# Kernel tuning notes

Measured on AMD Instinct MI355X. Metric: run time of the kernel, lower is better.

The kernel has to match this reference:

```python
import jax, jax.numpy as jnp
import numpy as np
from jax import lax

N, C_IN, C_OUT, H, W = 8, 64, 64, 128, 128
K, KS, STRIDE, PAD, GROUPS = 4, 3, 1, 1, 1


def setup_inputs() -> dict:
    key = jax.random.key(0)
    ks = jax.random.split(key, 10)
    s = 0.05
    return {
        "x": jax.random.normal(ks[0], (N, C_IN, H, W), jnp.float32),
        "weight": jax.random.normal(ks[1], (K, C_OUT, C_IN // GROUPS, KS, KS), jnp.float32) * s,
        "conv_w": jax.random.normal(ks[2], (C_OUT, C_IN, KS, KS), jnp.float32) * s,
        "conv_b": jax.random.normal(ks[3], (C_OUT,), jnp.float32) * s,
        "net0_w": jax.random.normal(ks[4], (K, 1, 1, 1, 1), jnp.float32) * s,
        "net0_b": jax.random.normal(ks[5], (K,), jnp.float32) * s,
        "net1_w": jax.random.normal(ks[6], (K, 1, 3, 3, 3), jnp.float32) * s,
        "net1_b": jax.random.normal(ks[7], (K,), jnp.float32) * s,
        "net2_w": jax.random.normal(ks[8], (K, 1, 5, 3, 3), jnp.float32) * s,
        "net2_b": jax.random.normal(ks[9], (K,), jnp.float32) * s,
    }


def _conv3d_mean(x5, w, b, pad):
    # x5: (N,1,C,H,W); w: (K,1,kd,kh,kw); 'same'-style padding per kernel.
    y = lax.conv_general_dilated(x5, w, (1, 1, 1), [(p, p) for p in pad],
                                 dimension_numbers=('NCDHW', 'OIDHW', 'NCDHW'))
    # global avg pool over (C,H,W); bias is constant so add after the mean.
    return jnp.mean(y, axis=(2, 3, 4)) + b[None, :]


def reference(x, weight, conv_w, conv_b, net0_w, net0_b, net1_w, net1_b, net2_w, net2_b):
    dn2 = ('NCHW', 'OIHW', 'NCHW')
    # static residual conv branch
    r = lax.conv_general_dilated(x, conv_w, (STRIDE, STRIDE), [(PAD, PAD)] * 2,
                                 dimension_numbers=dn2) + conv_b[None, :, None, None]
    # attention over 3D convs of x.unsqueeze(1)
    x5 = x[:, None]  # (N,1,C,H,W)
    logits = (_conv3d_mean(x5, net0_w, net0_b, (0, 0, 0))
              + _conv3d_mean(x5, net1_w, net1_b, (1, 1, 1))
              + _conv3d_mean(x5, net2_w, net2_b, (2, 1, 1)))  # (N,K)
    att = jax.nn.softmax(logits, axis=-1)
    # per-sample dynamic kernel mixing: (N,K) @ (K,out,in/g,kh,kw)
    agg_w = jnp.einsum('nk,koihw->noihw', att, weight)
    # grouped conv with groups = GROUPS*N == per-sample conv (vmapped)
    def per_sample(xi, wi):
        return lax.conv_general_dilated(xi[None], wi, (STRIDE, STRIDE), [(PAD, PAD)] * 2,
                                        dimension_numbers=dn2,
                                        feature_group_count=GROUPS)[0]
    out = jax.vmap(per_sample)(x, agg_w)  # (N,out,H,W)
    return out + r
```

## Files before the change

### kernel.cpp

```cpp
#include <hip/hip_runtime.h>


typedef unsigned short ushort_t;
typedef __attribute__((ext_vector_type(8))) short bf16x8;
typedef __attribute__((ext_vector_type(4))) float f32x4;

__device__ __forceinline__ ushort_t f2bf(float f) {
    unsigned u = __float_as_uint(f);
    unsigned r = (u + 0x7fffu + ((u >> 16) & 1u)) >> 16;
    return (ushort_t)r;
}

__global__ __launch_bounds__(256) void kTR(const float* __restrict__ x,
                                           ushort_t* __restrict__ xt,
                                           float* __restrict__ cat) {
    int bid = blockIdx.x;
    int h = bid & 127, n = bid >> 7;
    int tid = threadIdx.x;

    __shared__ ushort_t t[128 * 72];
    __shared__ float catloc[15];
    if (tid < 15) catloc[tid] = 0.f;
    __syncthreads();

    const float* xp = x + (size_t)n * 64 * 16384 + h * 128;
    int wq = tid & 31;

#pragma unroll
    for (int i = 0; i < 8; ++i) {
        int idx = i * 256 + tid;
        int ci = idx >> 5;
        float4 v = *(const float4*)(xp + (size_t)ci * 16384 + wq * 4);

        int w0 = wq * 4;
        t[(w0 + 0) * 72 + ci] = f2bf(v.x);
        t[(w0 + 1) * 72 + ci] = f2bf(v.y);
        t[(w0 + 2) * 72 + ci] = f2bf(v.z);
        t[(w0 + 3) * 72 + ci] = f2bf(v.w);

        float s4 = v.x + v.y + v.z + v.w;
#pragma unroll
        for (int m = 1; m <= 16; m <<= 1) s4 += __shfl_xor(s4, m);
        int cd = (ci == 0) ? 0 : (ci == 1) ? 1 : (ci == 62) ? 3 : (ci == 63) ? 4 : 2;
        if (wq == 0) {
            atomicAdd(&catloc[cd * 3 + 0], s4);
            atomicAdd(&catloc[cd * 3 + 1], v.x);
        }
        if (wq == 31) atomicAdd(&catloc[cd * 3 + 2], v.w);
    }
    __syncthreads();

    ushort_t* op = xt + ((size_t)(n * 128 + h)) * 128 * 64;
#pragma unroll
    for (int j = 0; j < 4; ++j) {
        int q = j * 256 + tid;
        int w = q >> 3, ci8 = q & 7;
        uint4 v = *(const uint4*)&t[w * 72 + ci8 * 8];
        *(uint4*)(op + (size_t)w * 64 + ci8 * 8) = v;
    }

    if (tid < 15) {
        int cd = tid / 3, st = tid % 3;
        int ch = (h == 0) ? 0 : (h == 127) ? 2 : 1;
        atomicAdd(&cat[((n * 5 + cd) * 3 + ch) * 3 + st], catloc[tid]);
    }
}

__global__ __launch_bounds__(256) void kW(const float* __restrict__ cat,
                                          const float* __restrict__ nw0, const float* __restrict__ nb0,
                                          const float* __restrict__ nw1, const float* __restrict__ nb1,
                                          const float* __restrict__ nw2, const float* __restrict__ nb2,
                                          const float* __restrict__ weight,
                                          const float* __restrict__ convw,
                                          ushort_t* __restrict__ weff) {
    int n = blockIdx.x >> 2, q = blockIdx.x & 3;
    int tid = threadIdx.x;
    __shared__ float att_s[4];

    if (tid < 4) {
        int k = tid;
        float c[5][3][3];
#pragma unroll
        for (int i = 0; i < 5; ++i)
#pragma unroll
            for (int j = 0; j < 3; ++j)
#pragma unroll
                for (int s = 0; s < 3; ++s)
                    c[i][j][s] = cat[((n * 5 + i) * 3 + j) * 3 + s];

        const float invV = 1.0f / (64.f * 128.f * 128.f);
        auto box = [&](int sd, int sh, int sw) -> float {
            float acc = 0.f;
#pragma unroll
            for (int cd = 0; cd < 5; ++cd) {
                int dv = (cd == 0) ? 0 : (cd == 1) ? 1 : (cd == 3) ? 62 : (cd == 4) ? 63 : -1;
                bool incd = (dv < 0) || (dv >= sd && dv < 64 + sd);
#pragma unroll
                for (int ch = 0; ch < 3; ++ch) {
                    int hv = (ch == 0) ? 0 : (ch == 2) ? 127 : -1;
                    bool inch = (hv < 0) || (hv >= sh && hv < 128 + sh);
                    if (incd && inch) {
                        float v = c[cd][ch][0];
                        if (sw == -1) v -= c[cd][ch][2];
                        else if (sw == 1) v -= c[cd][ch][1];
                        acc += v;
                    }
                }
            }
            return acc;
        };

        float lg = nb0[k] + nb1[k] + nb2[k];
        {
            float tot = 0.f;
#pragma unroll
            for (int i = 0; i < 5; ++i)
#pragma unroll
                for (int j = 0; j < 3; ++j) tot += c[i][j][0];
            lg += nw0[k] * tot * invV;
        }
#pragma unroll
        for (int dz = 0; dz < 3; ++dz)
#pragma unroll
            for (int dy = 0; dy < 3; ++dy)
#pragma unroll
                for (int dx = 0; dx < 3; ++dx)
                    lg += nw1[k * 27 + dz * 9 + dy * 3 + dx] *
                          box(dz - 1, dy - 1, dx - 1) * invV;
#pragma unroll
        for (int dz = 0; dz < 5; ++dz)
#pragma unroll
            for (int dy = 0; dy < 3; ++dy)
#pragma unroll
                for (int dx = 0; dx < 3; ++dx)
                    lg += nw2[k * 45 + dz * 9 + dy * 3 + dx] *
                          box(dz - 2, dy - 1, dx - 1) * invV;

        float m = fmaxf(lg, __shfl_xor(lg, 1));
        m = fmaxf(m, __shfl_xor(m, 2));
        float e = __expf(lg - m);
        float ssum = e + __shfl_xor(e, 1);
        ssum += __shfl_xor(ssum, 2);
        att_s[k] = e / ssum;
    }
    __syncthreads();

    float a0 = att_s[0], a1 = att_s[1], a2 = att_s[2], a3 = att_s[3];
    int ci = tid & 63;
    int co_base = q * 16 + (tid >> 6) * 4;
#pragma unroll
    for (int p = 0; p < 4; ++p) {
        int co = co_base + p;
        const float* cw = convw + (size_t)(co * 64 + ci) * 9;
        const float* w0 = weight + (size_t)((0 * 64 + co) * 64 + ci) * 9;
        const float* w1 = weight + (size_t)((1 * 64 + co) * 64 + ci) * 9;
        const float* w2 = weight + (size_t)((2 * 64 + co) * 64 + ci) * 9;
        const float* w3 = weight + (size_t)((3 * 64 + co) * 64 + ci) * 9;
#pragma unroll
        for (int s = 0; s < 9; ++s) {
            float v = cw[s] + a0 * w0[s] + a1 * w1[s] + a2 * w2[s] + a3 * w3[s];
            weff[((size_t)(n * 9 + s) * 64 + co) * 64 + ci] = f2bf(v);
        }
    }
}

__global__ __launch_bounds__(256) void kC(const ushort_t* __restrict__ xt,
                                          const ushort_t* __restrict__ weff,
                                          const float* __restrict__ convb,
                                          float* __restrict__ out) {
    int bid = blockIdx.x;
    int wt = bid & 1;
    int hp = (bid >> 1) & 63;
    int n = bid >> 7;
    int h0 = hp * 2;
    int w0 = wt * 64;

    __shared__ __align__(16) ushort_t lds[4 * 66 * 72];

    int tid = threadIdx.x;
    int lane = tid & 63;
    int wave = tid >> 6;
    int kq = lane >> 4;
    int l15 = lane & 15;

    for (int idx = tid; idx < 2112; idx += 256) {
        int ci8 = idx & 7;
        int rc = idx >> 3;
        int c = rc % 66;
        int r = rc / 66;
        int hg = h0 + r - 1;
        int wg = w0 + c - 1;
        uint4 v = make_uint4(0u, 0u, 0u, 0u);
        if (hg >= 0 && hg < 128 && wg >= 0 && wg < 128) {
            v = *(const uint4*)(xt + (((size_t)n * 128 + hg) * 128 + wg) * 64 + ci8 * 8);
        }
        *(uint4*)&lds[(r * 66 + c) * 72 + ci8 * 8] = v;
    }

    int co_a = wave * 16 + l15;
    bf16x8 afrag[9][2];
#pragma unroll
    for (int s = 0; s < 9; ++s)
#pragma unroll
        for (int kc = 0; kc < 2; ++kc)
            afrag[s][kc] = *(const bf16x8*)(weff +
                ((size_t)((n * 9 + s) * 64 + co_a)) * 64 + kc * 32 + kq * 8);

    f32x4 acc[8];
#pragma unroll
    for (int nt = 0; nt < 8; ++nt) acc[nt] = (f32x4){0.f, 0.f, 0.f, 0.f};

    __syncthreads();

#pragma unroll
    for (int s = 0; s < 9; ++s) {
        int ky = s / 3, kx = s % 3;
#pragma unroll
        for (int kc = 0; kc < 2; ++kc) {
#pragma unroll
            for (int nt = 0; nt < 8; ++nt) {
                int r = nt >> 2;
                int wl = (nt & 3) * 16 + l15;
                bf16x8 bfrag = *(const bf16x8*)
                    &lds[((r + ky) * 66 + wl + kx) * 72 + kc * 32 + kq * 8];
                acc[nt] = __builtin_amdgcn_mfma_f32_16x16x32_bf16(
                    afrag[s][kc], bfrag, acc[nt], 0, 0, 0);
            }
        }
    }

#pragma unroll
    for (int nt = 0; nt < 8; ++nt) {
        int h = h0 + (nt >> 2);
        int w = w0 + (nt & 3) * 16 + l15;
#pragma unroll
        for (int reg = 0; reg < 4; ++reg) {
            int co = wave * 16 + kq * 4 + reg;
            float v = acc[nt][reg] + convb[co];
            out[(((size_t)n * 64 + co) * 128 + h) * 128 + w] = v;
        }
    }
}

extern "C" void kernel_launch(void* const* d_in, const int* in_sizes, int n_in,
                              void* d_out, int out_size, void* d_ws, size_t ws_size,
                              hipStream_t stream) {
    const float* x      = (const float*)d_in[0];
    const float* weight = (const float*)d_in[1];
    const float* conv_w = (const float*)d_in[2];
    const float* conv_b = (const float*)d_in[3];
    const float* n0w    = (const float*)d_in[4];
    const float* n0b    = (const float*)d_in[5];
    const float* n1w    = (const float*)d_in[6];
    const float* n1b    = (const float*)d_in[7];
    const float* n2w    = (const float*)d_in[8];
    const float* n2b    = (const float*)d_in[9];
    float* out = (float*)d_out;

    char* ws = (char*)d_ws;
    ushort_t* xt   = (ushort_t*)(ws);
    ushort_t* weff = (ushort_t*)(ws + 16777216);
    float*    cat  = (float*)(ws + 16777216 + 589824);

    hipMemsetAsync(cat, 0, 1440, stream);
    kTR<<<1024, 256, 0, stream>>>(x, xt, cat);
    kW<<<32, 256, 0, stream>>>(cat, n0w, n0b, n1w, n1b, n2w, n2b,
                               weight, conv_w, weff);
    kC<<<1024, 256, 0, stream>>>(xt, weff, conv_b, out);
}
```

Measured before the change: 143.2 us.

## Use channel-blocked bf16 layout for xt and parallelize weight mixing

The transposed input changes from NHWC to a channel-blocked [n][h][ci8][w][8] layout. The transpose kernel no longer needs an LDS staging pass, and the conv kernel's LDS tile becomes unpadded and is read with a new index pattern. The attention/weight-mixing kernel spreads the 45 box sums across threads instead of one thread per k. It also launches one block per (sample, tap) pair, which raises block count from 32 to 72. The new global read pattern in kTR (scalar loads strided by 32) and possible LDS bank conflicts in kC are the risks.

```diff
diff --git a/kernel.cpp b/kernel.cpp
--- a/kernel.cpp
+++ b/kernel.cpp
@@ -17,47 +17,49 @@
     int bid = blockIdx.x;
     int h = bid & 127, n = bid >> 7;
     int tid = threadIdx.x;
-
-    __shared__ ushort_t t[128 * 72];
+    int wg = tid & 31;
+    int ci8 = tid >> 5;
+
     __shared__ float catloc[15];
     if (tid < 15) catloc[tid] = 0.f;
     __syncthreads();
 
-    const float* xp = x + (size_t)n * 64 * 16384 + h * 128;
-    int wq = tid & 31;
-
-#pragma unroll
-    for (int i = 0; i < 8; ++i) {
-        int idx = i * 256 + tid;
-        int ci = idx >> 5;
-        float4 v = *(const float4*)(xp + (size_t)ci * 16384 + wq * 4);
-
-        int w0 = wq * 4;
-        t[(w0 + 0) * 72 + ci] = f2bf(v.x);
-        t[(w0 + 1) * 72 + ci] = f2bf(v.y);
-        t[(w0 + 2) * 72 + ci] = f2bf(v.z);
-        t[(w0 + 3) * 72 + ci] = f2bf(v.w);
-
-        float s4 = v.x + v.y + v.z + v.w;
-#pragma unroll
-        for (int m = 1; m <= 16; m <<= 1) s4 += __shfl_xor(s4, m);
+    const float* xp = x + (size_t)(n * 64 + ci8 * 8) * 16384 + h * 128 + wg;
+    float v[8][4];
+#pragma unroll
+    for (int j = 0; j < 8; ++j)
+#pragma unroll
+        for (int c = 0; c < 4; ++c)
+            v[j][c] = xp[j * 16384 + c * 32];
+
+    ushort_t* op = xt + ((size_t)((n * 128 + h) * 8 + ci8)) * 128 * 8;
+#pragma unroll
+    for (int c = 0; c < 4; ++c) {
+        ushort_t u[8];
+#pragma unroll
+        for (int j = 0; j < 8; ++j) u[j] = f2bf(v[j][c]);
+        uint4 pk;
+        pk.x = (unsigned)u[0] | ((unsigned)u[1] << 16);
+        pk.y = (unsigned)u[2] | ((unsigned)u[3] << 16);
+        pk.z = (unsigned)u[4] | ((unsigned)u[5] << 16);
+        pk.w = (unsigned)u[6] | ((unsigned)u[7] << 16);
+        *(uint4*)(op + (size_t)(wg + c * 32) * 8) = pk;
+    }
+
+#pragma unroll
+    for (int j = 0; j < 8; ++j) {
+        float rs = v[j][0] + v[j][1] + v[j][2] + v[j][3];
+#pragma unroll
+        for (int m = 1; m <= 16; m <<= 1) rs += __shfl_xor(rs, m);
+        int ci = ci8 * 8 + j;
         int cd = (ci == 0) ? 0 : (ci == 1) ? 1 : (ci == 62) ? 3 : (ci == 63) ? 4 : 2;
-        if (wq == 0) {
-            atomicAdd(&catloc[cd * 3 + 0], s4);
-            atomicAdd(&catloc[cd * 3 + 1], v.x);
-        }
-        if (wq == 31) atomicAdd(&catloc[cd * 3 + 2], v.w);
-    }
-    __syncthreads();
-
-    ushort_t* op = xt + ((size_t)(n * 128 + h)) * 128 * 64;
-#pragma unroll
-    for (int j = 0; j < 4; ++j) {
-        int q = j * 256 + tid;
-        int w = q >> 3, ci8 = q & 7;
-        uint4 v = *(const uint4*)&t[w * 72 + ci8 * 8];
-        *(uint4*)(op + (size_t)w * 64 + ci8 * 8) = v;
-    }
+        if (wg == 0) {
+            atomicAdd(&catloc[cd * 3 + 0], rs);
+            atomicAdd(&catloc[cd * 3 + 1], v[j][0]);
+        }
+        if (wg == 31) atomicAdd(&catloc[cd * 3 + 2], v[j][3]);
+    }
+    __syncthreads();
 
     if (tid < 15) {
         int cd = tid / 3, st = tid % 3;
@@ -73,52 +75,62 @@
                                           const float* __restrict__ weight,
                                           const float* __restrict__ convw,
                                           ushort_t* __restrict__ weff) {
-    int n = blockIdx.x >> 2, q = blockIdx.x & 3;
+    int bid = blockIdx.x;
+    int s = bid % 9;
+    int n = bid / 9;
     int tid = threadIdx.x;
+
+    __shared__ float box_s[45];
+    __shared__ float tot_s;
     __shared__ float att_s[4];
 
-    if (tid < 4) {
-        int k = tid;
+    if (tid < 46) {
         float c[5][3][3];
 #pragma unroll
         for (int i = 0; i < 5; ++i)
 #pragma unroll
             for (int j = 0; j < 3; ++j)
 #pragma unroll
-                for (int s = 0; s < 3; ++s)
-                    c[i][j][s] = cat[((n * 5 + i) * 3 + j) * 3 + s];
-
-        const float invV = 1.0f / (64.f * 128.f * 128.f);
-        auto box = [&](int sd, int sh, int sw) -> float {
+                for (int t = 0; t < 3; ++t)
+                    c[i][j][t] = cat[((n * 5 + i) * 3 + j) * 3 + t];
+
+        if (tid < 45) {
+            int dz = tid / 9 - 2;
+            int dy = (tid / 3) % 3 - 1;
+            int dx = tid % 3 - 1;
             float acc = 0.f;
 #pragma unroll
             for (int cd = 0; cd < 5; ++cd) {
                 int dv = (cd == 0) ? 0 : (cd == 1) ? 1 : (cd == 3) ? 62 : (cd == 4) ? 63 : -1;
-                bool incd = (dv < 0) || (dv >= sd && dv < 64 + sd);
+                bool incd = (dv < 0) || (dv >= dz && dv < 64 + dz);
 #pragma unroll
                 for (int ch = 0; ch < 3; ++ch) {
                     int hv = (ch == 0) ? 0 : (ch == 2) ? 127 : -1;
-                    bool inch = (hv < 0) || (hv >= sh && hv < 128 + sh);
+                    bool inch = (hv < 0) || (hv >= dy && hv < 128 + dy);
                     if (incd && inch) {
                         float v = c[cd][ch][0];
-                        if (sw == -1) v -= c[cd][ch][2];
-                        else if (sw == 1) v -= c[cd][ch][1];
+                        if (dx == -1) v -= c[cd][ch][2];
+                        else if (dx == 1) v -= c[cd][ch][1];
                         acc += v;
                     }
                 }
             }
-            return acc;
-        };
-
-        float lg = nb0[k] + nb1[k] + nb2[k];
-        {
+            box_s[tid] = acc;
+        } else {
             float tot = 0.f;
 #pragma unroll
             for (int i = 0; i < 5; ++i)
 #pragma unroll
                 for (int j = 0; j < 3; ++j) tot += c[i][j][0];
-            lg += nw0[k] * tot * invV;
-        }
+            tot_s = tot;
+        }
+    }
+    __syncthreads();
+
+    if (tid < 4) {
+        int k = tid;
+        const float invV = 1.0f / (64.f * 128.f * 128.f);
+        float lg = nb0[k] + nb1[k] + nb2[k] + nw0[k] * tot_s * invV;
 #pragma unroll
         for (int dz = 0; dz < 3; ++dz)
 #pragma unroll
@@ -126,15 +138,10 @@
 #pragma unroll
                 for (int dx = 0; dx < 3; ++dx)
                     lg += nw1[k * 27 + dz * 9 + dy * 3 + dx] *
-                          box(dz - 1, dy - 1, dx - 1) * invV;
-#pragma unroll
-        for (int dz = 0; dz < 5; ++dz)
-#pragma unroll
-            for (int dy = 0; dy < 3; ++dy)
-#pragma unroll
-                for (int dx = 0; dx < 3; ++dx)
-                    lg += nw2[k * 45 + dz * 9 + dy * 3 + dx] *
-                          box(dz - 2, dy - 1, dx - 1) * invV;
+                          box_s[(dz + 1) * 9 + dy * 3 + dx] * invV;
+#pragma unroll
+        for (int b = 0; b < 45; ++b)
+            lg += nw2[k * 45 + b] * box_s[b] * invV;
 
         float m = fmaxf(lg, __shfl_xor(lg, 1));
         m = fmaxf(m, __shfl_xor(m, 2));
@@ -147,20 +154,18 @@
 
     float a0 = att_s[0], a1 = att_s[1], a2 = att_s[2], a3 = att_s[3];
     int ci = tid & 63;
-    int co_base = q * 16 + (tid >> 6) * 4;
-#pragma unroll
-    for (int p = 0; p < 4; ++p) {
-        int co = co_base + p;
-        const float* cw = convw + (size_t)(co * 64 + ci) * 9;
-        const float* w0 = weight + (size_t)((0 * 64 + co) * 64 + ci) * 9;
-        const float* w1 = weight + (size_t)((1 * 64 + co) * 64 + ci) * 9;
-        const float* w2 = weight + (size_t)((2 * 64 + co) * 64 + ci) * 9;
-        const float* w3 = weight + (size_t)((3 * 64 + co) * 64 + ci) * 9;
-#pragma unroll
-        for (int s = 0; s < 9; ++s) {
-            float v = cw[s] + a0 * w0[s] + a1 * w1[s] + a2 * w2[s] + a3 * w3[s];
-            weff[((size_t)(n * 9 + s) * 64 + co) * 64 + ci] = f2bf(v);
-        }
+    int cog = tid >> 6;
+    ushort_t* wp = weff + ((size_t)(n * 9 + s) * 64) * 64;
+#pragma unroll
+    for (int p = 0; p < 16; ++p) {
+        int co = cog * 16 + p;
+        size_t base = (size_t)(co * 64 + ci) * 9 + s;
+        float v = convw[base]
+                + a0 * weight[base]
+                + a1 * weight[base +     64 * 64 * 9]
+                + a2 * weight[base + 2 * 64 * 64 * 9]
+                + a3 * weight[base + 3 * 64 * 64 * 9];
+        wp[(size_t)co * 64 + ci] = f2bf(v);
     }
 }
 
@@ -175,7 +180,7 @@
     int h0 = hp * 2;
     int w0 = wt * 64;
 
-    __shared__ __align__(16) ushort_t lds[4 * 66 * 72];
+    __shared__ __align__(16) ushort_t lds[4 * 8 * 66 * 8];
 
     int tid = threadIdx.x;
     int lane = tid & 63;
@@ -184,17 +189,15 @@
     int l15 = lane & 15;
 
     for (int idx = tid; idx < 2112; idx += 256) {
-        int ci8 = idx & 7;
-        int rc = idx >> 3;
-        int c = rc % 66;
-        int r = rc / 66;
+        int c = idx % 66;
+        int rc8 = idx / 66;
+        int r = rc8 >> 3, ci8 = rc8 & 7;
         int hg = h0 + r - 1;
         int wg = w0 + c - 1;
-        uint4 v = make_uint4(0u, 0u, 0u, 0u);
-        if (hg >= 0 && hg < 128 && wg >= 0 && wg < 128) {
-            v = *(const uint4*)(xt + (((size_t)n * 128 + hg) * 128 + wg) * 64 + ci8 * 8);
-        }
-        *(uint4*)&lds[(r * 66 + c) * 72 + ci8 * 8] = v;
+        uint4 vv = make_uint4(0u, 0u, 0u, 0u);
+        if (hg >= 0 && hg < 128 && wg >= 0 && wg < 128)
+            vv = *(const uint4*)(xt + ((size_t)((n * 128 + hg) * 8 + ci8) * 128 + wg) * 8);
+        *(uint4*)&lds[(size_t)idx * 8] = vv;
     }
 
     int co_a = wave * 16 + l15;
@@ -222,7 +225,7 @@
                 int r = nt >> 2;
                 int wl = (nt & 3) * 16 + l15;
                 bf16x8 bfrag = *(const bf16x8*)
-                    &lds[((r + ky) * 66 + wl + kx) * 72 + kc * 32 + kq * 8];
+                    &lds[((((r + ky) * 8 + kc * 4 + kq) * 66) + wl + kx) * 8];
                 acc[nt] = __builtin_amdgcn_mfma_f32_16x16x32_bf16(
                     afrag[s][kc], bfrag, acc[nt], 0, 0, 0);
             }
@@ -264,7 +267,7 @@
 
     hipMemsetAsync(cat, 0, 1440, stream);
     kTR<<<1024, 256, 0, stream>>>(x, xt, cat);
-    kW<<<32, 256, 0, stream>>>(cat, n0w, n0b, n1w, n1b, n2w, n2b,
+    kW<<<72, 256, 0, stream>>>(cat, n0w, n0b, n1w, n1b, n2w, n2b,
                                weight, conv_w, weff);
     kC<<<1024, 256, 0, stream>>>(xt, weff, conv_b, out);
 }
```

After: 135.3 us. -5.6%, faster.
